# Performance work log

Hardware: AMD Instinct MI355X
Metric: run time of the kernel (lower is better)

The kernel has to match this reference:

```python
import jax, jax.numpy as jnp
import numpy as np

DIM = 2048
HID = 5632
ZERO_POINT = 128.0


def _qlinear(x, wq, scale):
    # wq: uint8-style codes stored as int32, shape [out, in]; scale: [out]
    W = (wq.astype(jnp.float32) - ZERO_POINT) * scale[:, None]  # dequant [out, in]
    return jnp.einsum('bsd,hd->bsh', x, W)


def setup_inputs() -> dict:
    key = jax.random.key(0)
    ks = jax.random.split(key, 7)
    B, S = 4, 2048
    # scale chosen so dequantized weights have ~1/sqrt(fan_in) magnitude
    sg = jax.random.uniform(ks[1], (HID,)) * (0.02 / np.sqrt(DIM)) + 1e-4
    su = jax.random.uniform(ks[3], (HID,)) * (0.02 / np.sqrt(DIM)) + 1e-4
    sd = jax.random.uniform(ks[5], (DIM,)) * (0.02 / np.sqrt(HID)) + 1e-4
    return {
        'x': jax.random.normal(ks[0], (B, S, DIM), dtype=jnp.float32),
        'wq_gate': jax.random.randint(ks[2], (HID, DIM), 0, 256, dtype=jnp.int32),
        's_gate': sg,
        'wq_up': jax.random.randint(ks[4], (HID, DIM), 0, 256, dtype=jnp.int32),
        's_up': su,
        'wq_down': jax.random.randint(ks[6], (DIM, HID), 0, 256, dtype=jnp.int32),
        's_down': sd,
    }


def reference(x, wq_gate, s_gate, wq_up, s_up, wq_down, s_down):
    gate = _qlinear(x, wq_gate, s_gate)          # [B, S, HID]
    gate = jax.nn.silu(gate)
    up = _qlinear(x, wq_up, s_up)                # [B, S, HID]
    return _qlinear(gate * up, wq_down, s_down)  # [B, S, DIM]
```

## Files before the change

### kernel.cpp

```cpp
#include <hip/hip_runtime.h>
#include <hip/hip_bf16.h>
#include <stdint.h>

#define DIM 2048
#define HID 5632

typedef __attribute__((ext_vector_type(8))) short short8;
typedef __attribute__((ext_vector_type(4))) float f32x4;
typedef __attribute__((ext_vector_type(4))) int int4v;
typedef __attribute__((ext_vector_type(4))) unsigned short ushort4v;

__device__ __forceinline__ unsigned short f32_to_bf16_rne(float f) {
    union { float f; unsigned u; } v; v.f = f;
    unsigned u = v.u;
    return (unsigned short)((u + 0x7FFFu + ((u >> 16) & 1u)) >> 16);
}

__device__ __forceinline__ void gload16(const void* g, void* l) {
    __builtin_amdgcn_global_load_lds(
        (const __attribute__((address_space(1))) void*)g,
        (__attribute__((address_space(3))) void*)l,
        16, 0, 0);
}

__global__ void dequant_plain(const int* __restrict__ wq, const float* __restrict__ scale,
                              unsigned short* __restrict__ out, long total, int cols) {
    long n4 = total >> 2;
    long stride = (long)gridDim.x * blockDim.x;
    for (long i = (long)blockIdx.x * blockDim.x + threadIdx.x; i < n4; i += stride) {
        int4v c = ((const int4v*)wq)[i];
        int row = (int)((i << 2) / cols);
        float s = scale[row];
        ushort4v o;
        o.x = f32_to_bf16_rne(((float)c.x - 128.0f) * s);
        o.y = f32_to_bf16_rne(((float)c.y - 128.0f) * s);
        o.z = f32_to_bf16_rne(((float)c.z - 128.0f) * s);
        o.w = f32_to_bf16_rne(((float)c.w - 128.0f) * s);
        ((ushort4v*)out)[i] = o;
    }
}

__global__ void dequant_gateup(const int* __restrict__ wg, const float* __restrict__ sg,
                               const int* __restrict__ wu, const float* __restrict__ su,
                               unsigned short* __restrict__ out) {
    const long n4 = (long)HID * DIM / 4;
    long stride = (long)gridDim.x * blockDim.x;
    for (long i = (long)blockIdx.x * blockDim.x + threadIdx.x; i < n4; i += stride) {
        int r  = (int)(i >> 9);
        int c4 = (int)(i & 511);
        int rp = ((r >> 4) << 5) + (r & 15);
        float s1 = sg[r], s2 = su[r];
        int4v g = ((const int4v*)wg)[i];
        int4v u = ((const int4v*)wu)[i];
        ushort4v og, ou;
        og.x = f32_to_bf16_rne(((float)g.x - 128.0f) * s1);
        og.y = f32_to_bf16_rne(((float)g.y - 128.0f) * s1);
        og.z = f32_to_bf16_rne(((float)g.z - 128.0f) * s1);
        og.w = f32_to_bf16_rne(((float)g.w - 128.0f) * s1);
        ou.x = f32_to_bf16_rne(((float)u.x - 128.0f) * s2);
        ou.y = f32_to_bf16_rne(((float)u.y - 128.0f) * s2);
        ou.z = f32_to_bf16_rne(((float)u.z - 128.0f) * s2);
        ou.w = f32_to_bf16_rne(((float)u.w - 128.0f) * s2);
        ((ushort4v*)out)[(long)rp * 512 + c4]        = og;
        ((ushort4v*)out)[(long)(rp + 16) * 512 + c4] = ou;
    }
}

__global__ void cast_f32_bf16(const float* __restrict__ in, unsigned short* __restrict__ out, long n) {
    long n4 = n >> 2;
    long stride = (long)gridDim.x * blockDim.x;
    for (long i = (long)blockIdx.x * blockDim.x + threadIdx.x; i < n4; i += stride) {
        f32x4 v = ((const f32x4*)in)[i];
        ushort4v o;
        o.x = f32_to_bf16_rne(v[0]);
        o.y = f32_to_bf16_rne(v[1]);
        o.z = f32_to_bf16_rne(v[2]);
        o.w = f32_to_bf16_rne(v[3]);
        ((ushort4v*)out)[i] = o;
    }
}


__global__ __launch_bounds__(512, 2) void gemm_gateup(
    const unsigned short* __restrict__ X,
    const unsigned short* __restrict__ Wp,
    unsigned short* __restrict__ H)
{
    __shared__ __attribute__((aligned(16))) unsigned short As[2][256 * 64];
    __shared__ __attribute__((aligned(16))) unsigned short Bs[2][256 * 64];

    const int tid  = threadIdx.x;
    const int lane = tid & 63;
    const int wid  = tid >> 6;
    const int wr   = wid >> 2;
    const int wc   = wid & 3;
    const int m0   = blockIdx.x << 8;
    const int n0   = blockIdx.y << 8;
    const int lr   = lane & 15;
    const int kg   = lane >> 4;

    int srow[4], skc[4], sdst[4];
    #pragma unroll
    for (int l = 0; l < 4; ++l) {
        int q = l * 512 + tid;
        srow[l] = q >> 3;
        skc[l]  = (((q & 7) ^ ((q >> 3) & 7)) << 3);
        sdst[l] = q << 3;
    }

    auto STAGE = [&](int buf, int kt) {
        const int kk = kt << 6;
        #pragma unroll
        for (int l = 0; l < 4; ++l) {
            gload16(X  + (size_t)(m0 + srow[l]) * DIM + kk + skc[l], &As[buf][sdst[l]]);
            gload16(Wp + (size_t)(n0 + srow[l]) * DIM + kk + skc[l], &Bs[buf][sdst[l]]);
        }
    };

    f32x4 acc[8][4];
    #pragma unroll
    for (int m = 0; m < 8; ++m)
        #pragma unroll
        for (int n = 0; n < 4; ++n) acc[m][n] = (f32x4){0.f, 0.f, 0.f, 0.f};

    const int c0 = ((kg ^ (lr & 7)) << 3);
    const int c1 = (((4 + kg) ^ (lr & 7)) << 3);
    const int abase = (wr * 128 + lr) * 64;
    const int bbase = (wc * 64 + lr) * 64;

    STAGE(0, 0);
    STAGE(1, 1);

    const int NT = DIM / 64;
    for (int kt = 0; kt < NT; ++kt) {
        const int cur = kt & 1;
        if (kt < NT - 1) asm volatile("s_waitcnt vmcnt(8)" ::: "memory");
        else             asm volatile("s_waitcnt vmcnt(0)" ::: "memory");
        __builtin_amdgcn_s_barrier();
        __builtin_amdgcn_sched_barrier(0);

        const unsigned short* ap0 = &As[cur][abase + c0];
        const unsigned short* ap1 = &As[cur][abase + c1];
        const unsigned short* bp0 = &Bs[cur][bbase + c0];
        const unsigned short* bp1 = &Bs[cur][bbase + c1];

        short8 a0[8], a1[8], b0[4], b1[4];
        #pragma unroll
        for (int n = 0; n < 4; ++n) {
            b0[n] = *(const short8*)(bp0 + (n << 10));
            b1[n] = *(const short8*)(bp1 + (n << 10));
        }
        #pragma unroll
        for (int m = 0; m < 8; ++m) {
            a0[m] = *(const short8*)(ap0 + (m << 10));
            a1[m] = *(const short8*)(ap1 + (m << 10));
        }

        __builtin_amdgcn_s_setprio(1);
        #pragma unroll
        for (int m = 0; m < 8; ++m)
            #pragma unroll
            for (int n = 0; n < 4; ++n)
                acc[m][n] = __builtin_amdgcn_mfma_f32_16x16x32_bf16(a0[m], b0[n], acc[m][n], 0, 0, 0);
        __builtin_amdgcn_s_setprio(0);
        __builtin_amdgcn_s_setprio(1);
        #pragma unroll
        for (int m = 0; m < 8; ++m)
            #pragma unroll
            for (int n = 0; n < 4; ++n)
                acc[m][n] = __builtin_amdgcn_mfma_f32_16x16x32_bf16(a1[m], b1[n], acc[m][n], 0, 0, 0);
        __builtin_amdgcn_s_setprio(0);

        __builtin_amdgcn_sched_barrier(0);
        __builtin_amdgcn_s_barrier();
        __builtin_amdgcn_sched_barrier(0);
        if (kt + 2 < NT) STAGE(cur, kt + 2);
        __builtin_amdgcn_sched_barrier(0);
    }

    const int lg = lane >> 4;
    #pragma unroll
    for (int m = 0; m < 8; ++m) {
        #pragma unroll
        for (int i = 0; i < 2; ++i) {
            f32x4 g = acc[m][2 * i], u = acc[m][2 * i + 1];
            const int col = (blockIdx.y << 7) + wc * 32 + i * 16 + lr;
            #pragma unroll
            for (int e = 0; e < 4; ++e) {
                const int row = m0 + wr * 128 + m * 16 + lg * 4 + e;
                float gv = g[e];
                float sg = gv / (1.0f + __expf(-gv));
                H[(size_t)row * HID + col] = f32_to_bf16_rne(sg * u[e]);
            }
        }
    }
}

__global__ __launch_bounds__(512, 2) void gemm_down(
    const unsigned short* __restrict__ Hb,
    const unsigned short* __restrict__ Wd,
    float* __restrict__ Out)
{
    __shared__ __attribute__((aligned(16))) unsigned short As[2][256 * 64];
    __shared__ __attribute__((aligned(16))) unsigned short Bs[2][256 * 64];

    const int tid  = threadIdx.x;
    const int lane = tid & 63;
    const int wid  = tid >> 6;
    const int wr   = wid >> 2;
    const int wc   = wid & 3;
    const int m0   = blockIdx.x << 8;
    const int n0   = blockIdx.y << 8;
    const int lr   = lane & 15;
    const int kg   = lane >> 4;

    int srow[4], skc[4], sdst[4];
    #pragma unroll
    for (int l = 0; l < 4; ++l) {
        int q = l * 512 + tid;
        srow[l] = q >> 3;
        skc[l]  = (((q & 7) ^ ((q >> 3) & 7)) << 3);
        sdst[l] = q << 3;
    }

    auto STAGE = [&](int buf, int kt) {
        const int kk = kt << 6;
        #pragma unroll
        for (int l = 0; l < 4; ++l) {
            gload16(Hb + (size_t)(m0 + srow[l]) * HID + kk + skc[l], &As[buf][sdst[l]]);
            gload16(Wd + (size_t)(n0 + srow[l]) * HID + kk + skc[l], &Bs[buf][sdst[l]]);
        }
    };

    f32x4 acc[8][4];
    #pragma unroll
    for (int m = 0; m < 8; ++m)
        #pragma unroll
        for (int n = 0; n < 4; ++n) acc[m][n] = (f32x4){0.f, 0.f, 0.f, 0.f};

    const int c0 = ((kg ^ (lr & 7)) << 3);
    const int c1 = (((4 + kg) ^ (lr & 7)) << 3);
    const int abase = (wr * 128 + lr) * 64;
    const int bbase = (wc * 64 + lr) * 64;

    STAGE(0, 0);
    STAGE(1, 1);

    const int NT = HID / 64;
    for (int kt = 0; kt < NT; ++kt) {
        const int cur = kt & 1;
        if (kt < NT - 1) asm volatile("s_waitcnt vmcnt(8)" ::: "memory");
        else             asm volatile("s_waitcnt vmcnt(0)" ::: "memory");
        __builtin_amdgcn_s_barrier();
        __builtin_amdgcn_sched_barrier(0);

        const unsigned short* ap0 = &As[cur][abase + c0];
        const unsigned short* ap1 = &As[cur][abase + c1];
        const unsigned short* bp0 = &Bs[cur][bbase + c0];
        const unsigned short* bp1 = &Bs[cur][bbase + c1];

        short8 a0[8], a1[8], b0[4], b1[4];
        #pragma unroll
        for (int n = 0; n < 4; ++n) {
            b0[n] = *(const short8*)(bp0 + (n << 10));
            b1[n] = *(const short8*)(bp1 + (n << 10));
        }
        #pragma unroll
        for (int m = 0; m < 8; ++m) {
            a0[m] = *(const short8*)(ap0 + (m << 10));
            a1[m] = *(const short8*)(ap1 + (m << 10));
        }

        __builtin_amdgcn_s_setprio(1);
        #pragma unroll
        for (int m = 0; m < 8; ++m)
            #pragma unroll
            for (int n = 0; n < 4; ++n)
                acc[m][n] = __builtin_amdgcn_mfma_f32_16x16x32_bf16(a0[m], b0[n], acc[m][n], 0, 0, 0);
        __builtin_amdgcn_s_setprio(0);
        __builtin_amdgcn_s_setprio(1);
        #pragma unroll
        for (int m = 0; m < 8; ++m)
            #pragma unroll
            for (int n = 0; n < 4; ++n)
                acc[m][n] = __builtin_amdgcn_mfma_f32_16x16x32_bf16(a1[m], b1[n], acc[m][n], 0, 0, 0);
        __builtin_amdgcn_s_setprio(0);

        __builtin_amdgcn_sched_barrier(0);
        __builtin_amdgcn_s_barrier();
        __builtin_amdgcn_sched_barrier(0);
        if (kt + 2 < NT) STAGE(cur, kt + 2);
        __builtin_amdgcn_sched_barrier(0);
    }

    const int lg = lane >> 4;
    #pragma unroll
    for (int m = 0; m < 8; ++m) {
        #pragma unroll
        for (int n = 0; n < 4; ++n) {
            const int col = n0 + wc * 64 + n * 16 + lr;
            #pragma unroll
            for (int e = 0; e < 4; ++e) {
                const int row = m0 + wr * 128 + m * 16 + lg * 4 + e;
                Out[(size_t)row * DIM + col] = acc[m][n][e];
            }
        }
    }
}

extern "C" void kernel_launch(void* const* d_in, const int* in_sizes, int n_in,
                              void* d_out, int out_size, void* d_ws, size_t ws_size,
                              hipStream_t stream) {
    const float* x      = (const float*)d_in[0];
    const int* wq_gate  = (const int*)d_in[1];
    const float* s_gate = (const float*)d_in[2];
    const int* wq_up    = (const int*)d_in[3];
    const float* s_up   = (const float*)d_in[4];
    const int* wq_down  = (const int*)d_in[5];
    const float* s_down = (const float*)d_in[6];
    float* out = (float*)d_out;

    const int M = in_sizes[0] / DIM;

    unsigned short* xb  = (unsigned short*)d_ws;
    unsigned short* wgu = xb + (size_t)M * DIM;
    unsigned short* h   = wgu + (size_t)2 * HID * DIM;

    cast_f32_bf16<<<2048, 256, 0, stream>>>(x, xb, (long)M * DIM);
    dequant_gateup<<<2048, 256, 0, stream>>>(wq_gate, s_gate, wq_up, s_up, wgu);

    gemm_gateup<<<dim3(M / 256, (2 * HID) / 256), 512, 0, stream>>>(xb, wgu, h);

    dequant_plain<<<2048, 256, 0, stream>>>(wq_down, s_down, wgu, (long)DIM * HID, HID);

    gemm_down<<<dim3(M / 256, DIM / 256), 512, 0, stream>>>(h, wgu, out);
}
```

Baseline: 587.7 us.

## Split GEMM K-step into four barrier-separated LDS-read/MFMA phases

Each 64-wide K tile in both GEMM kernels is now processed in four phases. Each phase loads a small set of A/B fragments from LDS, then runs a 4x4 block of MFMAs, with workgroup barriers and an lgkmcnt wait between phases. The intent is to lower the peak register count for fragments and to stagger LDS reads against matrix math across waves, in the style of ping-pong scheduling. The cost is many more barriers per iteration, which could stall waves and reduce overlap.

```diff
diff --git a/kernel.cpp b/kernel.cpp
--- a/kernel.cpp
+++ b/kernel.cpp
@@ -22,6 +22,18 @@
         (__attribute__((address_space(3))) void*)l,
         16, 0, 0);
 }
+
+#define PHASE_BEGIN \
+    __builtin_amdgcn_sched_barrier(0); \
+    __builtin_amdgcn_s_barrier(); \
+    asm volatile("s_waitcnt lgkmcnt(0)" ::: "memory"); \
+    __builtin_amdgcn_sched_barrier(0); \
+    __builtin_amdgcn_s_setprio(1);
+#define PHASE_END \
+    __builtin_amdgcn_s_setprio(0); \
+    __builtin_amdgcn_sched_barrier(0); \
+    __builtin_amdgcn_s_barrier(); \
+    __builtin_amdgcn_sched_barrier(0);
 
 __global__ void dequant_plain(const int* __restrict__ wq, const float* __restrict__ scale,
                               unsigned short* __restrict__ out, long total, int cols) {
@@ -136,6 +148,7 @@
         const int cur = kt & 1;
         if (kt < NT - 1) asm volatile("s_waitcnt vmcnt(8)" ::: "memory");
         else             asm volatile("s_waitcnt vmcnt(0)" ::: "memory");
+        __builtin_amdgcn_sched_barrier(0);
         __builtin_amdgcn_s_barrier();
         __builtin_amdgcn_sched_barrier(0);
 
@@ -144,36 +157,54 @@
         const unsigned short* bp0 = &Bs[cur][bbase + c0];
         const unsigned short* bp1 = &Bs[cur][bbase + c1];
 
-        short8 a0[8], a1[8], b0[4], b1[4];
-        #pragma unroll
-        for (int n = 0; n < 4; ++n) {
-            b0[n] = *(const short8*)(bp0 + (n << 10));
-            b1[n] = *(const short8*)(bp1 + (n << 10));
-        }
-        #pragma unroll
-        for (int m = 0; m < 8; ++m) {
-            a0[m] = *(const short8*)(ap0 + (m << 10));
-            a1[m] = *(const short8*)(ap1 + (m << 10));
-        }
-
-        __builtin_amdgcn_s_setprio(1);
-        #pragma unroll
-        for (int m = 0; m < 8; ++m)
+        short8 b0[4], a0[4];
+        #pragma unroll
+        for (int n = 0; n < 4; ++n) b0[n] = *(const short8*)(bp0 + (n << 10));
+        #pragma unroll
+        for (int m = 0; m < 4; ++m) a0[m] = *(const short8*)(ap0 + (m << 10));
+        PHASE_BEGIN
+        #pragma unroll
+        for (int m = 0; m < 4; ++m)
             #pragma unroll
             for (int n = 0; n < 4; ++n)
                 acc[m][n] = __builtin_amdgcn_mfma_f32_16x16x32_bf16(a0[m], b0[n], acc[m][n], 0, 0, 0);
-        __builtin_amdgcn_s_setprio(0);
-        __builtin_amdgcn_s_setprio(1);
-        #pragma unroll
-        for (int m = 0; m < 8; ++m)
-            #pragma unroll
-            for (int n = 0; n < 4; ++n)
-                acc[m][n] = __builtin_amdgcn_mfma_f32_16x16x32_bf16(a1[m], b1[n], acc[m][n], 0, 0, 0);
-        __builtin_amdgcn_s_setprio(0);
-
-        __builtin_amdgcn_sched_barrier(0);
-        __builtin_amdgcn_s_barrier();
-        __builtin_amdgcn_sched_barrier(0);
+        PHASE_END
+
+        short8 a1[4];
+        #pragma unroll
+        for (int m = 0; m < 4; ++m) a1[m] = *(const short8*)(ap0 + ((m + 4) << 10));
+        PHASE_BEGIN
+        #pragma unroll
+        for (int m = 0; m < 4; ++m)
+            #pragma unroll
+            for (int n = 0; n < 4; ++n)
+                acc[m + 4][n] = __builtin_amdgcn_mfma_f32_16x16x32_bf16(a1[m], b0[n], acc[m + 4][n], 0, 0, 0);
+        PHASE_END
+
+        short8 b1[4], a2[4];
+        #pragma unroll
+        for (int n = 0; n < 4; ++n) b1[n] = *(const short8*)(bp1 + (n << 10));
+        #pragma unroll
+        for (int m = 0; m < 4; ++m) a2[m] = *(const short8*)(ap1 + (m << 10));
+        PHASE_BEGIN
+        #pragma unroll
+        for (int m = 0; m < 4; ++m)
+            #pragma unroll
+            for (int n = 0; n < 4; ++n)
+                acc[m][n] = __builtin_amdgcn_mfma_f32_16x16x32_bf16(a2[m], b1[n], acc[m][n], 0, 0, 0);
+        PHASE_END
+
+        short8 a3[4];
+        #pragma unroll
+        for (int m = 0; m < 4; ++m) a3[m] = *(const short8*)(ap1 + ((m + 4) << 10));
+        PHASE_BEGIN
+        #pragma unroll
+        for (int m = 0; m < 4; ++m)
+            #pragma unroll
+            for (int n = 0; n < 4; ++n)
+                acc[m + 4][n] = __builtin_amdgcn_mfma_f32_16x16x32_bf16(a3[m], b1[n], acc[m + 4][n], 0, 0, 0);
+        PHASE_END
+
         if (kt + 2 < NT) STAGE(cur, kt + 2);
         __builtin_amdgcn_sched_barrier(0);
     }
@@ -251,6 +282,7 @@
         const int cur = kt & 1;
         if (kt < NT - 1) asm volatile("s_waitcnt vmcnt(8)" ::: "memory");
         else             asm volatile("s_waitcnt vmcnt(0)" ::: "memory");
+        __builtin_amdgcn_sched_barrier(0);
         __builtin_amdgcn_s_barrier();
         __builtin_amdgcn_sched_barrier(0);
 
@@ -259,36 +291,54 @@
         const unsigned short* bp0 = &Bs[cur][bbase + c0];
         const unsigned short* bp1 = &Bs[cur][bbase + c1];
 
-        short8 a0[8], a1[8], b0[4], b1[4];
-        #pragma unroll
-        for (int n = 0; n < 4; ++n) {
-            b0[n] = *(const short8*)(bp0 + (n << 10));
-            b1[n] = *(const short8*)(bp1 + (n << 10));
-        }
-        #pragma unroll
-        for (int m = 0; m < 8; ++m) {
-            a0[m] = *(const short8*)(ap0 + (m << 10));
-            a1[m] = *(const short8*)(ap1 + (m << 10));
-        }
-
-        __builtin_amdgcn_s_setprio(1);
-        #pragma unroll
-        for (int m = 0; m < 8; ++m)
+        short8 b0[4], a0[4];
+        #pragma unroll
+        for (int n = 0; n < 4; ++n) b0[n] = *(const short8*)(bp0 + (n << 10));
+        #pragma unroll
+        for (int m = 0; m < 4; ++m) a0[m] = *(const short8*)(ap0 + (m << 10));
+        PHASE_BEGIN
+        #pragma unroll
+        for (int m = 0; m < 4; ++m)
             #pragma unroll
             for (int n = 0; n < 4; ++n)
                 acc[m][n] = __builtin_amdgcn_mfma_f32_16x16x32_bf16(a0[m], b0[n], acc[m][n], 0, 0, 0);
-        __builtin_amdgcn_s_setprio(0);
-        __builtin_amdgcn_s_setprio(1);
-        #pragma unroll
-        for (int m = 0; m < 8; ++m)
-            #pragma unroll
-            for (int n = 0; n < 4; ++n)
-                acc[m][n] = __builtin_amdgcn_mfma_f32_16x16x32_bf16(a1[m], b1[n], acc[m][n], 0, 0, 0);
-        __builtin_amdgcn_s_setprio(0);
-
-        __builtin_amdgcn_sched_barrier(0);
-        __builtin_amdgcn_s_barrier();
-        __builtin_amdgcn_sched_barrier(0);
+        PHASE_END
+
+        short8 a1[4];
+        #pragma unroll
+        for (int m = 0; m < 4; ++m) a1[m] = *(const short8*)(ap0 + ((m + 4) << 10));
+        PHASE_BEGIN
+        #pragma unroll
+        for (int m = 0; m < 4; ++m)
+            #pragma unroll
+            for (int n = 0; n < 4; ++n)
+                acc[m + 4][n] = __builtin_amdgcn_mfma_f32_16x16x32_bf16(a1[m], b0[n], acc[m + 4][n], 0, 0, 0);
+        PHASE_END
+
+        short8 b1[4], a2[4];
+        #pragma unroll
+        for (int n = 0; n < 4; ++n) b1[n] = *(const short8*)(bp1 + (n << 10));
+        #pragma unroll
+        for (int m = 0; m < 4; ++m) a2[m] = *(const short8*)(ap1 + (m << 10));
+        PHASE_BEGIN
+        #pragma unroll
+        for (int m = 0; m < 4; ++m)
+            #pragma unroll
+            for (int n = 0; n < 4; ++n)
+                acc[m][n] = __builtin_amdgcn_mfma_f32_16x16x32_bf16(a2[m], b1[n], acc[m][n], 0, 0, 0);
+        PHASE_END
+
+        short8 a3[4];
+        #pragma unroll
+        for (int m = 0; m < 4; ++m) a3[m] = *(const short8*)(ap1 + ((m + 4) << 10));
+        PHASE_BEGIN
+        #pragma unroll
+        for (int m = 0; m < 4; ++m)
+            #pragma unroll
+            for (int n = 0; n < 4; ++n)
+                acc[m + 4][n] = __builtin_amdgcn_mfma_f32_16x16x32_bf16(a3[m], b1[n], acc[m + 4][n], 0, 0, 0);
+        PHASE_END
+
         if (kt + 2 < NT) STAGE(cur, kt + 2);
         __builtin_amdgcn_sched_barrier(0);
     }
```

After: 664.7 us. +13.1%, slower.

## Restructure GEMM K-loop into four-phase ping-pong schedule with half-K staging

Applied to the files above, without the earlier changes.

Replaces the per-tile double-buffered loop in both GEMMs with a schedule that splits each 64-wide K tile into two 32-wide halves and interleaves LDS reads, async global-to-LDS loads and MFMA groups in four barrier-separated phases. The LDS layout changes to 32-element rows with a new XOR swizzle, and launch bounds drop to one block per CU. The aim is to overlap global loads with MFMA work more finely and lower LDS bank conflicts and register pressure. The cost is more barriers per K tile and lower occupancy.

```diff
diff --git a/kernel.cpp b/kernel.cpp
--- a/kernel.cpp
+++ b/kernel.cpp
@@ -22,6 +22,25 @@
         (__attribute__((address_space(3))) void*)l,
         16, 0, 0);
 }
+
+#define PH_OPEN \
+    __builtin_amdgcn_sched_barrier(0); \
+    __builtin_amdgcn_s_barrier(); \
+    asm volatile("s_waitcnt lgkmcnt(0)" ::: "memory"); \
+    __builtin_amdgcn_sched_barrier(0); \
+    __builtin_amdgcn_s_setprio(1);
+#define PH_CLOSE \
+    __builtin_amdgcn_s_setprio(0); \
+    __builtin_amdgcn_sched_barrier(0); \
+    __builtin_amdgcn_s_barrier(); \
+    __builtin_amdgcn_sched_barrier(0);
+#define PH_CLOSE_VM(N) \
+    __builtin_amdgcn_s_setprio(0); \
+    __builtin_amdgcn_sched_barrier(0); \
+    asm volatile("s_waitcnt vmcnt(" #N ")" ::: "memory"); \
+    __builtin_amdgcn_sched_barrier(0); \
+    __builtin_amdgcn_s_barrier(); \
+    __builtin_amdgcn_sched_barrier(0);
 
 __global__ void dequant_plain(const int* __restrict__ wq, const float* __restrict__ scale,
                               unsigned short* __restrict__ out, long total, int cols) {
@@ -81,102 +100,128 @@
 }
 
 
-__global__ __launch_bounds__(512, 2) void gemm_gateup(
+#define GEMM_PROLOGUE_COMMON(Aptr, Bptr, LDA, LDB)                                   \
+    const int tid  = threadIdx.x;                                                    \
+    const int lane = tid & 63;                                                       \
+    const int wid  = tid >> 6;                                                       \
+    const int wr   = wid >> 2;                                                       \
+    const int wc   = wid & 3;                                                        \
+    const int m0   = blockIdx.x << 8;                                                \
+    const int n0   = blockIdx.y << 8;                                                \
+    const int lr   = lane & 15;                                                      \
+    const int kg   = lane >> 4;                                                      \
+    const int ck   = ((kg ^ ((lr >> 1) & 3)) << 3);                                  \
+    const int aboff = (wr * 128 + lr) * 32;                                          \
+    const int bboff = (wc * 64 + lr) * 32;                                           \
+    int srow[2], scol[2], sdst[2];                                                   \
+    _Pragma("unroll")                                                                \
+    for (int l = 0; l < 2; ++l) {                                                    \
+        int p = tid + (l << 9);                                                      \
+        srow[l] = p >> 2;                                                            \
+        scol[l] = (((p & 3) ^ ((p >> 3) & 3)) << 3);                                 \
+        sdst[l] = p << 3;                                                            \
+    }                                                                                \
+    auto STAGE_A = [&](int t, int kh) {                                              \
+        if (t < NT) {                                                                \
+            unsigned short* dst = As + ((((t & 1) << 1) | kh) << 13);                \
+            _Pragma("unroll")                                                        \
+            for (int l = 0; l < 2; ++l)                                              \
+                gload16(Aptr + (size_t)(m0 + srow[l]) * LDA + (t << 6) + (kh << 5) + scol[l], \
+                        dst + sdst[l]);                                              \
+        }                                                                            \
+    };                                                                               \
+    auto STAGE_B = [&](int t, int kh) {                                              \
+        if (t < NT) {                                                                \
+            unsigned short* dst = Bs + ((((t & 1) << 1) | kh) << 13);                \
+            _Pragma("unroll")                                                        \
+            for (int l = 0; l < 2; ++l)                                              \
+                gload16(Bptr + (size_t)(n0 + srow[l]) * LDB + (t << 6) + (kh << 5) + scol[l], \
+                        dst + sdst[l]);                                              \
+        }                                                                            \
+    };                                                                               \
+    f32x4 acc[8][4];                                                                 \
+    _Pragma("unroll")                                                                \
+    for (int m = 0; m < 8; ++m)                                                      \
+        _Pragma("unroll")                                                            \
+        for (int n = 0; n < 4; ++n) acc[m][n] = (f32x4){0.f, 0.f, 0.f, 0.f};         \
+                            \
+    STAGE_A(0, 0); STAGE_B(0, 0);                                                    \
+    STAGE_A(0, 1); STAGE_B(0, 1);                                                    \
+    STAGE_A(1, 0); STAGE_B(1, 0);                                                    \
+    asm volatile("s_waitcnt vmcnt(8)" ::: "memory");                                 \
+    __builtin_amdgcn_s_barrier();
+
+#define GEMM_KLOOP_BODY                                                              \
+    for (int t = 0; t < NT; ++t) {                                                   \
+        const int buf = t & 1;                                                       \
+        const unsigned short* a0p = As + ((buf << 1) << 13) + aboff + ck;            \
+        const unsigned short* a1p = As + (((buf << 1) | 1) << 13) + aboff + ck;      \
+        const unsigned short* b0p = Bs + ((buf << 1) << 13) + bboff + ck;            \
+        const unsigned short* b1p = Bs + (((buf << 1) | 1) << 13) + bboff + ck;      \
+                                            \
+        short8 b0[4], aL0[4];                                                        \
+        _Pragma("unroll")                                                            \
+        for (int n = 0; n < 4; ++n) b0[n] = *(const short8*)(b0p + (n << 9));        \
+        _Pragma("unroll")                                                            \
+        for (int m = 0; m < 4; ++m) aL0[m] = *(const short8*)(a0p + (m << 9));       \
+        STAGE_A(t + 1, 1);                                                           \
+        PH_OPEN                                                                      \
+        _Pragma("unroll")                                                            \
+        for (int m = 0; m < 4; ++m)                                                  \
+            _Pragma("unroll")                                                        \
+            for (int n = 0; n < 4; ++n)                                              \
+                acc[m][n] = __builtin_amdgcn_mfma_f32_16x16x32_bf16(aL0[m], b0[n], acc[m][n], 0, 0, 0); \
+        PH_CLOSE                                                                     \
+                           \
+        short8 aH0[4];                                                               \
+        _Pragma("unroll")                                                            \
+        for (int m = 0; m < 4; ++m) aH0[m] = *(const short8*)(a0p + ((m + 4) << 9)); \
+        STAGE_B(t + 1, 1);                                                           \
+        PH_OPEN                                                                      \
+        _Pragma("unroll")                                                            \
+        for (int m = 0; m < 4; ++m)                                                  \
+            _Pragma("unroll")                                                        \
+            for (int n = 0; n < 4; ++n)                                              \
+                acc[m + 4][n] = __builtin_amdgcn_mfma_f32_16x16x32_bf16(aH0[m], b0[n], acc[m + 4][n], 0, 0, 0); \
+        if (t < NT - 1) { PH_CLOSE_VM(8) } else { PH_CLOSE_VM(0) }                   \
+                                            \
+        short8 b1[4], aL1[4];                                                        \
+        _Pragma("unroll")                                                            \
+        for (int n = 0; n < 4; ++n) b1[n] = *(const short8*)(b1p + (n << 9));        \
+        _Pragma("unroll")                                                            \
+        for (int m = 0; m < 4; ++m) aL1[m] = *(const short8*)(a1p + (m << 9));       \
+        STAGE_A(t + 2, 0);                                                           \
+        PH_OPEN                                                                      \
+        _Pragma("unroll")                                                            \
+        for (int m = 0; m < 4; ++m)                                                  \
+            _Pragma("unroll")                                                        \
+            for (int n = 0; n < 4; ++n)                                              \
+                acc[m][n] = __builtin_amdgcn_mfma_f32_16x16x32_bf16(aL1[m], b1[n], acc[m][n], 0, 0, 0); \
+        PH_CLOSE                                                                     \
+                         \
+        short8 aH1[4];                                                               \
+        _Pragma("unroll")                                                            \
+        for (int m = 0; m < 4; ++m) aH1[m] = *(const short8*)(a1p + ((m + 4) << 9)); \
+        STAGE_B(t + 2, 0);                                                           \
+        PH_OPEN                                                                      \
+        _Pragma("unroll")                                                            \
+        for (int m = 0; m < 4; ++m)                                                  \
+            _Pragma("unroll")                                                        \
+            for (int n = 0; n < 4; ++n)                                              \
+                acc[m + 4][n] = __builtin_amdgcn_mfma_f32_16x16x32_bf16(aH1[m], b1[n], acc[m + 4][n], 0, 0, 0); \
+        if (t < NT - 2) { PH_CLOSE_VM(8) } else { PH_CLOSE_VM(4) }                   \
+    }
+
+__global__ __launch_bounds__(512, 1) void gemm_gateup(
     const unsigned short* __restrict__ X,
     const unsigned short* __restrict__ Wp,
     unsigned short* __restrict__ H)
 {
-    __shared__ __attribute__((aligned(16))) unsigned short As[2][256 * 64];
-    __shared__ __attribute__((aligned(16))) unsigned short Bs[2][256 * 64];
-
-    const int tid  = threadIdx.x;
-    const int lane = tid & 63;
-    const int wid  = tid >> 6;
-    const int wr   = wid >> 2;
-    const int wc   = wid & 3;
-    const int m0   = blockIdx.x << 8;
-    const int n0   = blockIdx.y << 8;
-    const int lr   = lane & 15;
-    const int kg   = lane >> 4;
-
-    int srow[4], skc[4], sdst[4];
-    #pragma unroll
-    for (int l = 0; l < 4; ++l) {
-        int q = l * 512 + tid;
-        srow[l] = q >> 3;
-        skc[l]  = (((q & 7) ^ ((q >> 3) & 7)) << 3);
-        sdst[l] = q << 3;
-    }
-
-    auto STAGE = [&](int buf, int kt) {
-        const int kk = kt << 6;
-        #pragma unroll
-        for (int l = 0; l < 4; ++l) {
-            gload16(X  + (size_t)(m0 + srow[l]) * DIM + kk + skc[l], &As[buf][sdst[l]]);
-            gload16(Wp + (size_t)(n0 + srow[l]) * DIM + kk + skc[l], &Bs[buf][sdst[l]]);
-        }
-    };
-
-    f32x4 acc[8][4];
-    #pragma unroll
-    for (int m = 0; m < 8; ++m)
-        #pragma unroll
-        for (int n = 0; n < 4; ++n) acc[m][n] = (f32x4){0.f, 0.f, 0.f, 0.f};
-
-    const int c0 = ((kg ^ (lr & 7)) << 3);
-    const int c1 = (((4 + kg) ^ (lr & 7)) << 3);
-    const int abase = (wr * 128 + lr) * 64;
-    const int bbase = (wc * 64 + lr) * 64;
-
-    STAGE(0, 0);
-    STAGE(1, 1);
-
+    __shared__ __attribute__((aligned(16))) unsigned short As[2 * 2 * 8192];
+    __shared__ __attribute__((aligned(16))) unsigned short Bs[2 * 2 * 8192];
     const int NT = DIM / 64;
-    for (int kt = 0; kt < NT; ++kt) {
-        const int cur = kt & 1;
-        if (kt < NT - 1) asm volatile("s_waitcnt vmcnt(8)" ::: "memory");
-        else             asm volatile("s_waitcnt vmcnt(0)" ::: "memory");
-        __builtin_amdgcn_s_barrier();
-        __builtin_amdgcn_sched_barrier(0);
-
-        const unsigned short* ap0 = &As[cur][abase + c0];
-        const unsigned short* ap1 = &As[cur][abase + c1];
-        const unsigned short* bp0 = &Bs[cur][bbase + c0];
-        const unsigned short* bp1 = &Bs[cur][bbase + c1];
-
-        short8 a0[8], a1[8], b0[4], b1[4];
-        #pragma unroll
-        for (int n = 0; n < 4; ++n) {
-            b0[n] = *(const short8*)(bp0 + (n << 10));
-            b1[n] = *(const short8*)(bp1 + (n << 10));
-        }
-        #pragma unroll
-        for (int m = 0; m < 8; ++m) {
-            a0[m] = *(const short8*)(ap0 + (m << 10));
-            a1[m] = *(const short8*)(ap1 + (m << 10));
-        }
-
-        __builtin_amdgcn_s_setprio(1);
-        #pragma unroll
-        for (int m = 0; m < 8; ++m)
-            #pragma unroll
-            for (int n = 0; n < 4; ++n)
-                acc[m][n] = __builtin_amdgcn_mfma_f32_16x16x32_bf16(a0[m], b0[n], acc[m][n], 0, 0, 0);
-        __builtin_amdgcn_s_setprio(0);
-        __builtin_amdgcn_s_setprio(1);
-        #pragma unroll
-        for (int m = 0; m < 8; ++m)
-            #pragma unroll
-            for (int n = 0; n < 4; ++n)
-                acc[m][n] = __builtin_amdgcn_mfma_f32_16x16x32_bf16(a1[m], b1[n], acc[m][n], 0, 0, 0);
-        __builtin_amdgcn_s_setprio(0);
-
-        __builtin_amdgcn_sched_barrier(0);
-        __builtin_amdgcn_s_barrier();
-        __builtin_amdgcn_sched_barrier(0);
-        if (kt + 2 < NT) STAGE(cur, kt + 2);
-        __builtin_amdgcn_sched_barrier(0);
-    }
+    GEMM_PROLOGUE_COMMON(X, Wp, DIM, DIM)
+    GEMM_KLOOP_BODY
 
     const int lg = lane >> 4;
     #pragma unroll
@@ -196,102 +241,16 @@
     }
 }
 
-__global__ __launch_bounds__(512, 2) void gemm_down(
+__global__ __launch_bounds__(512, 1) void gemm_down(
     const unsigned short* __restrict__ Hb,
     const unsigned short* __restrict__ Wd,
     float* __restrict__ Out)
 {
-    __shared__ __attribute__((aligned(16))) unsigned short As[2][256 * 64];
-    __shared__ __attribute__((aligned(16))) unsigned short Bs[2][256 * 64];
-
-    const int tid  = threadIdx.x;
-    const int lane = tid & 63;
-    const int wid  = tid >> 6;
-    const int wr   = wid >> 2;
-    const int wc   = wid & 3;
-    const int m0   = blockIdx.x << 8;
-    const int n0   = blockIdx.y << 8;
-    const int lr   = lane & 15;
-    const int kg   = lane >> 4;
-
-    int srow[4], skc[4], sdst[4];
-    #pragma unroll
-    for (int l = 0; l < 4; ++l) {
-        int q = l * 512 + tid;
-        srow[l] = q >> 3;
-        skc[l]  = (((q & 7) ^ ((q >> 3) & 7)) << 3);
-        sdst[l] = q << 3;
-    }
-
-    auto STAGE = [&](int buf, int kt) {
-        const int kk = kt << 6;
-        #pragma unroll
-        for (int l = 0; l < 4; ++l) {
-            gload16(Hb + (size_t)(m0 + srow[l]) * HID + kk + skc[l], &As[buf][sdst[l]]);
-            gload16(Wd + (size_t)(n0 + srow[l]) * HID + kk + skc[l], &Bs[buf][sdst[l]]);
-        }
-    };
-
-    f32x4 acc[8][4];
-    #pragma unroll
-    for (int m = 0; m < 8; ++m)
-        #pragma unroll
-        for (int n = 0; n < 4; ++n) acc[m][n] = (f32x4){0.f, 0.f, 0.f, 0.f};
-
-    const int c0 = ((kg ^ (lr & 7)) << 3);
-    const int c1 = (((4 + kg) ^ (lr & 7)) << 3);
-    const int abase = (wr * 128 + lr) * 64;
-    const int bbase = (wc * 64 + lr) * 64;
-
-    STAGE(0, 0);
-    STAGE(1, 1);
-
+    __shared__ __attribute__((aligned(16))) unsigned short As[2 * 2 * 8192];
+    __shared__ __attribute__((aligned(16))) unsigned short Bs[2 * 2 * 8192];
     const int NT = HID / 64;
-    for (int kt = 0; kt < NT; ++kt) {
-        const int cur = kt & 1;
-        if (kt < NT - 1) asm volatile("s_waitcnt vmcnt(8)" ::: "memory");
-        else             asm volatile("s_waitcnt vmcnt(0)" ::: "memory");
-        __builtin_amdgcn_s_barrier();
-        __builtin_amdgcn_sched_barrier(0);
-
-        const unsigned short* ap0 = &As[cur][abase + c0];
-        const unsigned short* ap1 = &As[cur][abase + c1];
-        const unsigned short* bp0 = &Bs[cur][bbase + c0];
-        const unsigned short* bp1 = &Bs[cur][bbase + c1];
-
-        short8 a0[8], a1[8], b0[4], b1[4];
-        #pragma unroll
-        for (int n = 0; n < 4; ++n) {
-            b0[n] = *(const short8*)(bp0 + (n << 10));
-            b1[n] = *(const short8*)(bp1 + (n << 10));
-        }
-        #pragma unroll
-        for (int m = 0; m < 8; ++m) {
-            a0[m] = *(const short8*)(ap0 + (m << 10));
-            a1[m] = *(const short8*)(ap1 + (m << 10));
-        }
-
-        __builtin_amdgcn_s_setprio(1);
-        #pragma unroll
-        for (int m = 0; m < 8; ++m)
-            #pragma unroll
-            for (int n = 0; n < 4; ++n)
-                acc[m][n] = __builtin_amdgcn_mfma_f32_16x16x32_bf16(a0[m], b0[n], acc[m][n], 0, 0, 0);
-        __builtin_amdgcn_s_setprio(0);
-        __builtin_amdgcn_s_setprio(1);
-        #pragma unroll
-        for (int m = 0; m < 8; ++m)
-            #pragma unroll
-            for (int n = 0; n < 4; ++n)
-                acc[m][n] = __builtin_amdgcn_mfma_f32_16x16x32_bf16(a1[m], b1[n], acc[m][n], 0, 0, 0);
-        __builtin_amdgcn_s_setprio(0);
-
-        __builtin_amdgcn_sched_barrier(0);
-        __builtin_amdgcn_s_barrier();
-        __builtin_amdgcn_sched_barrier(0);
-        if (kt + 2 < NT) STAGE(cur, kt + 2);
-        __builtin_amdgcn_sched_barrier(0);
-    }
+    GEMM_PROLOGUE_COMMON(Hb, Wd, HID, HID)
+    GEMM_KLOOP_BODY
 
     const int lg = lane >> 4;
     #pragma unroll
```

Result: no change. 597.8 us (+1.7%).
